# Kernel tuning notes

Measured on AMD Instinct MI355X. Metric: run time of the kernel, lower is better.

Reference implementation:

```python
import jax, jax.numpy as jnp
import numpy as np

B, N, D, H = 256, 40, 256, 256      # molecules, atoms/molecule, pc_hidden, pred_hidden
nS, nC, nB = 40, 5, 5               # n_SYMBOLS, n_FORMAL_CHARGES, n_BOND_TYPES
NEG_SLOPE = 0.01                    # F.leaky_relu default


def _lrelu(x):
    return jnp.where(x >= 0, x, NEG_SLOPE * x)


def setup_inputs() -> dict:
    key = jax.random.key(0)
    ks = jax.random.split(key, 7)
    def w(k, shape, fan_in):
        return jax.random.normal(k, shape, jnp.float32) / np.float32(np.sqrt(fan_in))
    return {
        "yhat": jax.random.normal(ks[0], (B, N, D), jnp.float32),
        "Ws1": w(ks[1], (D, H), D),      "bs1": jnp.zeros((H,), jnp.float32),
        "Ws2": w(ks[2], (H, nS), H),     "bs2": jnp.zeros((nS,), jnp.float32),
        "Wc1": w(ks[3], (D, H), D),      "bc1": jnp.zeros((H,), jnp.float32),
        "Wc2": w(ks[4], (H, nC), H),     "bc2": jnp.zeros((nC,), jnp.float32),
        "Wb1": w(ks[5], (2 * D, H), 2 * D), "bb1": jnp.zeros((H,), jnp.float32),
        "Wb2": w(ks[6], (H, nB), H),     "bb2": jnp.zeros((nB,), jnp.float32),
    }


def reference(yhat, Ws1, bs1, Ws2, bs2, Wc1, bc1, Wc2, bc2, Wb1, bb1, Wb2, bb2):
    # Per-atom symbol / charge heads (2-layer MLP with leaky_relu)
    symbols = _lrelu(yhat @ Ws1 + bs1) @ Ws2 + bs2          # [B, N, nS]
    charges = _lrelu(yhat @ Wc1 + bc1) @ Wc2 + bc2          # [B, N, nC]

    # Pairwise bond head: concat(x_i, x_j) @ Wb1 == x_i @ Wb1[:D] + x_j @ Wb1[D:]
    # (avoids materializing the [B, N, N, 2D] concat tensor)
    p1 = yhat @ Wb1[:D]                                      # [B, N, H]
    p2 = yhat @ Wb1[D:]                                      # [B, N, H]
    h = _lrelu(p1[:, :, None, :] + p2[:, None, :, :] + bb1)  # [B, N, N, H]
    bonds = h @ Wb2 + bb2                                    # [B, N, N, nB]
    bonds = bonds + jnp.swapaxes(bonds, 1, 2)                # symmetrize (i,j)+(j,i)

    return (symbols.reshape(-1, nS),
            charges.reshape(-1, nC),
            bonds.reshape(-1, nB))
```

## Files before the change

### kernel.cpp

```cpp
#include <hip/hip_runtime.h>
#include <hip/hip_bf16.h>

typedef unsigned short u16;
typedef __attribute__((ext_vector_type(4))) int   int4v;
typedef __attribute__((ext_vector_type(4))) unsigned int uint4v;
typedef __attribute__((ext_vector_type(4))) unsigned short ushort4v;
typedef __attribute__((ext_vector_type(4))) float floatx4;
typedef __attribute__((ext_vector_type(8))) short bf16x8;

#define LRELU_NS 0.01f
#define SK 264

__device__ __forceinline__ float bitsToF(unsigned int b) {
    union { unsigned int u; float f; } v; v.u = b << 16; return v.f;
}
__device__ __forceinline__ float bfLo(unsigned int d) {
    union { unsigned int u; float f; } v; v.u = d << 16; return v.f;
}
__device__ __forceinline__ float bfHi(unsigned int d) {
    union { unsigned int u; float f; } v; v.u = d & 0xffff0000u; return v.f;
}
__device__ __forceinline__ u16 f2bf(float f) {
    __hip_bfloat16 h = __float2bfloat16(f);
    return *reinterpret_cast<u16*>(&h);
}
__device__ __forceinline__ float lrelu(float v) {
    return fmaxf(v, LRELU_NS * v);
}
__device__ __forceinline__ u16 ldW(const void* p, int i, int isF32) {
    return isF32 ? f2bf(((const float*)p)[i]) : ((const u16*)p)[i];
}
__device__ __forceinline__ float ldF(const void* p, int i, int isF32) {
    return isF32 ? ((const float*)p)[i]
                 : bitsToF((unsigned int)((const u16*)p)[i]);
}

__device__ __forceinline__ int computeIsF32(const u16* y, int* cnt, int t) {
    if (t == 0) *cnt = 0;
    __syncthreads();
    if (t < 256) {
        u16 v = y[2 * t];
        int e = (v >> 7) & 0xFF;
        if (v == 0 || (e >= 96 && e < 160)) atomicAdd(cnt, 1);
    }
    __syncthreads();
    return (*cnt < 192) ? 1 : 0;
}

__global__ __launch_bounds__(256) void pack_kernel(
    const void* __restrict__ yhat,
    const void* __restrict__ Ws1, const void* __restrict__ Wc1,
    const void* __restrict__ Wb1, const void* __restrict__ Ws2,
    const void* __restrict__ Wc2,
    const void* __restrict__ bs1, const void* __restrict__ bc1,
    const void* __restrict__ bb1, const void* __restrict__ bs2,
    const void* __restrict__ bc2, const void* __restrict__ bb2,
    u16* __restrict__ WallT, u16* __restrict__ W2T, float* __restrict__ biasF)
{
    __shared__ int fcnt;
    const int bid = blockIdx.x, t = threadIdx.x;
    const int isF32 = computeIsF32((const u16*)yhat, &fcnt, t);
    if (bid < 64) {
        __shared__ u16 tile[64][65];
        const int c0 = (bid & 15) * 64;
        const int k0 = (bid >> 4) * 64;
        const void* src; int coff; int roff = 0;
        if (c0 < 256)      { src = Ws1; coff = c0; }
        else if (c0 < 512) { src = Wc1; coff = c0 - 256; }
        else if (c0 < 768) { src = Wb1; coff = c0 - 512; }
        else               { src = Wb1; coff = c0 - 768; roff = 256; }
        const int cc = t & 63, kk0 = t >> 6;
        #pragma unroll
        for (int i = 0; i < 16; ++i) {
            int kk = kk0 + i * 4;
            tile[kk][cc] = ldW(src, (k0 + kk + roff) * 256 + coff + cc, isF32);
        }
        __syncthreads();
        const int kk2 = t & 63, cc0 = t >> 6;
        #pragma unroll
        for (int i = 0; i < 16; ++i) {
            int cc2 = cc0 + i * 4;
            WallT[(c0 + cc2) * 256 + (k0 + kk2)] = tile[kk2][cc2];
        }
    } else if (bid < 128) {
        int e2 = (bid - 64) * 256 + t;
        int c = e2 >> 8, k = e2 & 255;
        u16 v = 0;
        if (c < 40)                 v = ldW(Ws2, k * 40 + c, isF32);
        else if (c >= 48 && c < 53) v = ldW(Wc2, k * 5 + (c - 48), isF32);
        W2T[c * 256 + k] = v;
    } else {
        int idx = (bid - 128) * 256 + t;
        float v = 0.f;
        if (idx < 256)       v = ldF(bs1, idx, isF32);
        else if (idx < 512)  v = ldF(bc1, idx - 256, isF32);
        else if (idx < 768)  v = ldF(bb1, idx - 512, isF32);
        else if (idx < 808)  v = ldF(bs2, idx - 768, isF32);
        else if (idx < 813)  v = ldF(bc2, idx - 808, isF32);
        else if (idx >= 816 && idx < 821) v = ldF(bb2, idx - 816, isF32);
        biasF[idx] = v;
    }
}

__global__ __launch_bounds__(512) void heads2_kernel(
    const void* __restrict__ Xv, const u16* __restrict__ WallT,
    const u16* __restrict__ W2T, const float* __restrict__ biasF,
    void* __restrict__ outv)
{
    __shared__ u16 Xs[64 * SK];
    __shared__ u16 Hb[64 * SK];
    __shared__ int fcnt;
    const int t = threadIdx.x;
    const int bm0 = blockIdx.x * 64;
    const int head = blockIdx.y;
    const int isF32 = computeIsF32((const u16*)Xv, &fcnt, t);

    if (isF32) {
        const floatx4* __restrict__ src = (const floatx4*)((const float*)Xv + bm0 * 256);
        #pragma unroll
        for (int s = 0; s < 8; ++s) {
            int cid = t + s * 512;
            int row = cid >> 6, ch = cid & 63;
            floatx4 f = src[cid];
            ushort4v u;
            u[0] = f2bf(f[0]); u[1] = f2bf(f[1]); u[2] = f2bf(f[2]); u[3] = f2bf(f[3]);
            *(ushort4v*)&Xs[row * SK + ch * 4] = u;
        }
    } else {
        const int4v* __restrict__ src = (const int4v*)((const u16*)Xv + bm0 * 256);
        #pragma unroll
        for (int s = 0; s < 4; ++s) {
            int cid = t + s * 512;
            int row = cid >> 5, ch = cid & 31;
            *(int4v*)&Xs[row * SK + ch * 8] = src[cid];
        }
    }
    __syncthreads();

    const int w = t >> 6, l = t & 63;
    const int ml = l & 15, kq = l >> 4, r0 = kq * 4;

    #pragma unroll
    for (int n = 0; n < 2; ++n) {
        const int ct = w + 8 * n;
        floatx4 acc[4] = {};
        #pragma unroll
        for (int ks = 0; ks < 8; ++ks) {
            const int k0 = ks * 32 + kq * 8;
            bf16x8 bf = *(const bf16x8*)&WallT[(head * 256 + ct * 16 + ml) * 256 + k0];
            #pragma unroll
            for (int mt = 0; mt < 4; ++mt) {
                bf16x8 a = *(const bf16x8*)&Xs[(mt * 16 + ml) * SK + k0];
                acc[mt] = __builtin_amdgcn_mfma_f32_16x16x32_bf16(a, bf, acc[mt], 0, 0, 0);
            }
        }
        const int col = ct * 16 + ml;
        const float bias = biasF[head * 256 + col];
        #pragma unroll
        for (int mt = 0; mt < 4; ++mt)
            #pragma unroll
            for (int r = 0; r < 4; ++r)
                Hb[(mt * 16 + r0 + r) * SK + col] = f2bf(lrelu(acc[mt][r] + bias));
    }
    __syncthreads();

    if (w < 4) {
        const int nct = (head == 0) ? 3 : 1;
        const int c0  = (head == 0) ? 0 : 48;
        floatx4 acc2[3] = {};
        #pragma unroll
        for (int ks = 0; ks < 8; ++ks) {
            const int k0 = ks * 32 + kq * 8;
            bf16x8 a = *(const bf16x8*)&Hb[(w * 16 + ml) * SK + k0];
            #pragma unroll
            for (int j = 0; j < 3; ++j) {
                if (j < nct) {
                    bf16x8 bf = *(const bf16x8*)&W2T[(c0 + j * 16 + ml) * 256 + k0];
                    acc2[j] = __builtin_amdgcn_mfma_f32_16x16x32_bf16(a, bf, acc2[j], 0, 0, 0);
                }
            }
        }
        #pragma unroll
        for (int j = 0; j < 3; ++j) {
            if (j < nct) {
                const int col = j * 16 + ml;
                const int lim = (head == 0) ? 40 : 5;
                if (col < lim) {
                    const float bias = biasF[(head == 0 ? 768 : 808) + col];
                    #pragma unroll
                    for (int r = 0; r < 4; ++r) {
                        const int row = bm0 + w * 16 + r0 + r;
                        const int o = (head == 0) ? row * 40 + col
                                                  : 409600 + row * 5 + col;
                        const float v = acc2[j][r] + bias;
                        if (isF32) ((float*)outv)[o] = v;
                        else ((__hip_bfloat16*)outv)[o] = __float2bfloat16(v);
                    }
                }
            }
        }
    }
}

__global__ __launch_bounds__(512) void bonds2_kernel(
    const void* __restrict__ Xv, const u16* __restrict__ WallT,
    const void* __restrict__ Wb2, const float* __restrict__ biasF,
    void* __restrict__ outv)
{
    __shared__ u16 Xm[48 * SK];
    __shared__ u16 P1L[48 * SK];
    __shared__ u16 P2L[48 * SK];
    __shared__ u16 WsB[5 * 264];
    __shared__ int fcnt;
    const int t = threadIdx.x, b = blockIdx.x;
    const int isF32 = computeIsF32((const u16*)Xv, &fcnt, t);

    if (isF32) {
        const floatx4* __restrict__ src = (const floatx4*)((const float*)Xv + b * 10240);
        #pragma unroll
        for (int s = 0; s < 5; ++s) {
            int cid = t + s * 512;
            int row = cid >> 6, ch = cid & 63;
            floatx4 f = src[cid];
            ushort4v u;
            u[0] = f2bf(f[0]); u[1] = f2bf(f[1]); u[2] = f2bf(f[2]); u[3] = f2bf(f[3]);
            *(ushort4v*)&Xm[row * SK + ch * 4] = u;
        }
        {
            int row = 40 + (t >> 6), ch = t & 63;
            ushort4v z = {0, 0, 0, 0};
            *(ushort4v*)&Xm[row * SK + ch * 4] = z;
        }
    } else {
        const int4v* __restrict__ src = (const int4v*)((const u16*)Xv + b * 10240);
        #pragma unroll
        for (int s = 0; s < 3; ++s) {
            int cid = t + s * 512;
            int row = cid >> 5, ch = cid & 31;
            if (cid < 1280) *(int4v*)&Xm[row * SK + ch * 8] = src[cid];
            else { int4v z = {0, 0, 0, 0}; *(int4v*)&Xm[row * SK + ch * 8] = z; }
        }
    }
    #pragma unroll
    for (int s = 0; s < 3; ++s) {
        int e2 = t + s * 512;
        if (e2 < 1280) {
            int c = e2 >> 8, k = e2 & 255;
            WsB[c * 264 + k] = ldW(Wb2, k * 5 + c, isF32);
        }
    }
    __syncthreads();

    const int w = t >> 6, l = t & 63;
    const int ml = l & 15, kq = l >> 4, r0 = kq * 4;

    for (int n = 0; n < 4; ++n) {
        const int gc = (w + 8 * n) * 16 + ml;
        floatx4 acc[3] = {};
        #pragma unroll
        for (int ks = 0; ks < 8; ++ks) {
            const int k0 = ks * 32 + kq * 8;
            bf16x8 bf = *(const bf16x8*)&WallT[(512 + gc) * 256 + k0];
            #pragma unroll
            for (int i = 0; i < 3; ++i) {
                bf16x8 a = *(const bf16x8*)&Xm[(i * 16 + ml) * SK + k0];
                acc[i] = __builtin_amdgcn_mfma_f32_16x16x32_bf16(a, bf, acc[i], 0, 0, 0);
            }
        }
        u16* dst = (gc < 256) ? P1L : P2L;
        const int col = gc & 255;
        const float bias = (gc < 256) ? biasF[512 + gc] : 0.f;
        #pragma unroll
        for (int i = 0; i < 3; ++i)
            #pragma unroll
            for (int r = 0; r < 4; ++r)
                dst[(i * 16 + r0 + r) * SK + col] = f2bf(acc[i][r] + bias);
    }
    __syncthreads();

    const int sel = (ml < 5) ? ml : 4;
    bf16x8 wf[8];
    #pragma unroll
    for (int ks = 0; ks < 8; ++ks)
        wf[ks] = *(const bf16x8*)&WsB[sel * 264 + ks * 32 + kq * 8];
    const float b2x2 = 2.f * biasF[816 + ml];

    for (int m = 0; m < 5; ++m) {
        const int i = w + 8 * m;
        const int itile = i >> 4;
        for (int jt = itile; jt < 3; ++jt) {
            floatx4 accF = {}, accB = {};
            #pragma unroll
            for (int ks = 0; ks < 8; ++ks) {
                const int k0 = ks * 32 + kq * 8;
                const uint4v a1 = *(const uint4v*)&P1L[i * SK + k0];
                const uint4v a2 = *(const uint4v*)&P2L[i * SK + k0];
                const uint4v b1 = *(const uint4v*)&P1L[(jt * 16 + ml) * SK + k0];
                const uint4v b2 = *(const uint4v*)&P2L[(jt * 16 + ml) * SK + k0];
                bf16x8 afF, afB;
                #pragma unroll
                for (int d = 0; d < 4; ++d) {
                    afF[2 * d]     = (short)f2bf(lrelu(bfLo(a1[d]) + bfLo(b2[d])));
                    afF[2 * d + 1] = (short)f2bf(lrelu(bfHi(a1[d]) + bfHi(b2[d])));
                    afB[2 * d]     = (short)f2bf(lrelu(bfLo(b1[d]) + bfLo(a2[d])));
                    afB[2 * d + 1] = (short)f2bf(lrelu(bfHi(b1[d]) + bfHi(a2[d])));
                }
                accF = __builtin_amdgcn_mfma_f32_16x16x32_bf16(afF, wf[ks], accF, 0, 0, 0);
                accB = __builtin_amdgcn_mfma_f32_16x16x32_bf16(afB, wf[ks], accB, 0, 0, 0);
            }
            if (ml < 5) {
                const bool diag = (jt == itile);
                #pragma unroll
                for (int r = 0; r < 4; ++r) {
                    const int j = jt * 16 + r0 + r;
                    if (j < 40 && (!diag || j >= i)) {
                        const float v = accF[r] + accB[r] + b2x2;
                        const int o1 = 460800 + (b * 1600 + i * 40 + j) * 5 + ml;
                        if (isF32) ((float*)outv)[o1] = v;
                        else ((__hip_bfloat16*)outv)[o1] = __float2bfloat16(v);
                        if (!diag || j > i) {
                            const int o2 = 460800 + (b * 1600 + j * 40 + i) * 5 + ml;
                            if (isF32) ((float*)outv)[o2] = v;
                            else ((__hip_bfloat16*)outv)[o2] = __float2bfloat16(v);
                        }
                    }
                }
            }
        }
    }
}

extern "C" void kernel_launch(void* const* d_in, const int* in_sizes, int n_in,
                              void* d_out, int out_size, void* d_ws, size_t ws_size,
                              hipStream_t stream)
{
    const void* yhat = d_in[0];
    const void* Ws1  = d_in[1];
    const void* bs1  = d_in[2];
    const void* Ws2  = d_in[3];
    const void* bs2  = d_in[4];
    const void* Wc1  = d_in[5];
    const void* bc1  = d_in[6];
    const void* Wc2  = d_in[7];
    const void* bc2  = d_in[8];
    const void* Wb1  = d_in[9];
    const void* bb1  = d_in[10];
    const void* Wb2  = d_in[11];
    const void* bb2  = d_in[12];

    char* wsb = (char*)d_ws;
    float* biasF = (float*)(wsb + 4096);
    u16*   W2T   = (u16*)(wsb + 8192);
    u16*   WallT = (u16*)(wsb + 40960);

    pack_kernel<<<132, 256, 0, stream>>>(yhat, Ws1, Wc1, Wb1, Ws2, Wc2,
                                         bs1, bc1, bb1, bs2, bc2, bb2,
                                         WallT, W2T, biasF);
    heads2_kernel<<<dim3(160, 2), 512, 0, stream>>>(yhat, WallT, W2T, biasF, d_out);
    bonds2_kernel<<<256, 512, 0, stream>>>(yhat, WallT, Wb2, biasF, d_out);
}
```

Measured before the change: 146.5 us.

## Use packed fp16 math for bond hidden, merge F/B MFMAs, split bonds blocks

The bond kernel now stores P1/P2 and Wb2 in fp16 and computes the pairwise add and leaky-relu with packed half2 arithmetic. It sums the forward and backward activations before a single f16 MFMA, which halves the MFMA count per tile. Each molecule's tile pairs are spread over two blocks so the grid doubles to 512, trading a repeat of the P1/P2 projection per block for more parallelism. The heads kernel drops to 256 threads with all waves taking part in the second layer; fp16 has less range than bf16, so large activations could lose accuracy.

```diff
diff --git a/kernel.cpp b/kernel.cpp
--- a/kernel.cpp
+++ b/kernel.cpp
@@ -7,18 +7,14 @@
 typedef __attribute__((ext_vector_type(4))) unsigned short ushort4v;
 typedef __attribute__((ext_vector_type(4))) float floatx4;
 typedef __attribute__((ext_vector_type(8))) short bf16x8;
+typedef _Float16 half8 __attribute__((ext_vector_type(8)));
+typedef _Float16 half2v __attribute__((ext_vector_type(2)));
 
 #define LRELU_NS 0.01f
 #define SK 264
 
 __device__ __forceinline__ float bitsToF(unsigned int b) {
     union { unsigned int u; float f; } v; v.u = b << 16; return v.f;
-}
-__device__ __forceinline__ float bfLo(unsigned int d) {
-    union { unsigned int u; float f; } v; v.u = d << 16; return v.f;
-}
-__device__ __forceinline__ float bfHi(unsigned int d) {
-    union { unsigned int u; float f; } v; v.u = d & 0xffff0000u; return v.f;
 }
 __device__ __forceinline__ u16 f2bf(float f) {
     __hip_bfloat16 h = __float2bfloat16(f);
@@ -33,6 +29,20 @@
 __device__ __forceinline__ float ldF(const void* p, int i, int isF32) {
     return isF32 ? ((const float*)p)[i]
                  : bitsToF((unsigned int)((const u16*)p)[i]);
+}
+__device__ __forceinline__ u16 f2h_bits(float f) {
+    union { _Float16 h; u16 u; } v; v.h = (_Float16)f; return v.u;
+}
+__device__ __forceinline__ u16 ldWh(const void* p, int i, int isF32) {
+    float f = isF32 ? ((const float*)p)[i]
+                    : bitsToF((unsigned int)((const u16*)p)[i]);
+    return f2h_bits(f);
+}
+__device__ __forceinline__ half2v u2h2(unsigned int x) {
+    union { unsigned int u; half2v h; } v; v.u = x; return v.h;
+}
+__device__ __forceinline__ unsigned int h22u(half2v x) {
+    union { half2v h; unsigned int u; } v; v.h = x; return v.u;
 }
 
 __device__ __forceinline__ int computeIsF32(const u16* y, int* cnt, int t) {
@@ -102,7 +112,7 @@
     }
 }
 
-__global__ __launch_bounds__(512) void heads2_kernel(
+__global__ __launch_bounds__(256) void heads_kernel(
     const void* __restrict__ Xv, const u16* __restrict__ WallT,
     const u16* __restrict__ W2T, const float* __restrict__ biasF,
     void* __restrict__ outv)
@@ -118,8 +128,8 @@
     if (isF32) {
         const floatx4* __restrict__ src = (const floatx4*)((const float*)Xv + bm0 * 256);
         #pragma unroll
-        for (int s = 0; s < 8; ++s) {
-            int cid = t + s * 512;
+        for (int it = 0; it < 16; ++it) {
+            int cid = t + it * 256;
             int row = cid >> 6, ch = cid & 63;
             floatx4 f = src[cid];
             ushort4v u;
@@ -129,8 +139,8 @@
     } else {
         const int4v* __restrict__ src = (const int4v*)((const u16*)Xv + bm0 * 256);
         #pragma unroll
-        for (int s = 0; s < 4; ++s) {
-            int cid = t + s * 512;
+        for (int it = 0; it < 8; ++it) {
+            int cid = t + it * 256;
             int row = cid >> 5, ch = cid & 31;
             *(int4v*)&Xs[row * SK + ch * 8] = src[cid];
         }
@@ -140,9 +150,8 @@
     const int w = t >> 6, l = t & 63;
     const int ml = l & 15, kq = l >> 4, r0 = kq * 4;
 
-    #pragma unroll
-    for (int n = 0; n < 2; ++n) {
-        const int ct = w + 8 * n;
+    for (int n = 0; n < 4; ++n) {
+        const int ct = w + 4 * n;
         floatx4 acc[4] = {};
         #pragma unroll
         for (int ks = 0; ks < 8; ++ks) {
@@ -164,45 +173,43 @@
     }
     __syncthreads();
 
-    if (w < 4) {
-        const int nct = (head == 0) ? 3 : 1;
-        const int c0  = (head == 0) ? 0 : 48;
-        floatx4 acc2[3] = {};
-        #pragma unroll
-        for (int ks = 0; ks < 8; ++ks) {
-            const int k0 = ks * 32 + kq * 8;
-            bf16x8 a = *(const bf16x8*)&Hb[(w * 16 + ml) * SK + k0];
-            #pragma unroll
-            for (int j = 0; j < 3; ++j) {
-                if (j < nct) {
-                    bf16x8 bf = *(const bf16x8*)&W2T[(c0 + j * 16 + ml) * 256 + k0];
-                    acc2[j] = __builtin_amdgcn_mfma_f32_16x16x32_bf16(a, bf, acc2[j], 0, 0, 0);
-                }
-            }
-        }
+    const int nct = (head == 0) ? 3 : 1;
+    const int c0  = (head == 0) ? 0 : 48;
+    floatx4 acc2[3] = {};
+    #pragma unroll
+    for (int ks = 0; ks < 8; ++ks) {
+        const int k0 = ks * 32 + kq * 8;
+        bf16x8 a = *(const bf16x8*)&Hb[(w * 16 + ml) * SK + k0];
         #pragma unroll
         for (int j = 0; j < 3; ++j) {
             if (j < nct) {
-                const int col = j * 16 + ml;
-                const int lim = (head == 0) ? 40 : 5;
-                if (col < lim) {
-                    const float bias = biasF[(head == 0 ? 768 : 808) + col];
-                    #pragma unroll
-                    for (int r = 0; r < 4; ++r) {
-                        const int row = bm0 + w * 16 + r0 + r;
-                        const int o = (head == 0) ? row * 40 + col
-                                                  : 409600 + row * 5 + col;
-                        const float v = acc2[j][r] + bias;
-                        if (isF32) ((float*)outv)[o] = v;
-                        else ((__hip_bfloat16*)outv)[o] = __float2bfloat16(v);
-                    }
+                bf16x8 bf = *(const bf16x8*)&W2T[(c0 + j * 16 + ml) * 256 + k0];
+                acc2[j] = __builtin_amdgcn_mfma_f32_16x16x32_bf16(a, bf, acc2[j], 0, 0, 0);
+            }
+        }
+    }
+    #pragma unroll
+    for (int j = 0; j < 3; ++j) {
+        if (j < nct) {
+            const int col = j * 16 + ml;
+            const int lim = (head == 0) ? 40 : 5;
+            if (col < lim) {
+                const float bias = biasF[(head == 0 ? 768 : 808) + col];
+                #pragma unroll
+                for (int r = 0; r < 4; ++r) {
+                    const int row = bm0 + w * 16 + r0 + r;
+                    const int o = (head == 0) ? row * 40 + col
+                                              : 409600 + row * 5 + col;
+                    const float v = acc2[j][r] + bias;
+                    if (isF32) ((float*)outv)[o] = v;
+                    else ((__hip_bfloat16*)outv)[o] = __float2bfloat16(v);
                 }
             }
         }
     }
 }
 
-__global__ __launch_bounds__(512) void bonds2_kernel(
+__global__ __launch_bounds__(512) void bonds3_kernel(
     const void* __restrict__ Xv, const u16* __restrict__ WallT,
     const void* __restrict__ Wb2, const float* __restrict__ biasF,
     void* __restrict__ outv)
@@ -212,7 +219,9 @@
     __shared__ u16 P2L[48 * SK];
     __shared__ u16 WsB[5 * 264];
     __shared__ int fcnt;
-    const int t = threadIdx.x, b = blockIdx.x;
+    const int t = threadIdx.x;
+    const int b = blockIdx.x >> 1;
+    const int h = blockIdx.x & 1;
     const int isF32 = computeIsF32((const u16*)Xv, &fcnt, t);
 
     if (isF32) {
@@ -246,7 +255,7 @@
         int e2 = t + s * 512;
         if (e2 < 1280) {
             int c = e2 >> 8, k = e2 & 255;
-            WsB[c * 264 + k] = ldW(Wb2, k * 5 + c, isF32);
+            WsB[c * 264 + k] = ldWh(Wb2, k * 5 + c, isF32);
         }
     }
     __syncthreads();
@@ -274,55 +283,58 @@
         for (int i = 0; i < 3; ++i)
             #pragma unroll
             for (int r = 0; r < 4; ++r)
-                dst[(i * 16 + r0 + r) * SK + col] = f2bf(acc[i][r] + bias);
+                dst[(i * 16 + r0 + r) * SK + col] = f2h_bits(acc[i][r] + bias);
     }
     __syncthreads();
 
     const int sel = (ml < 5) ? ml : 4;
-    bf16x8 wf[8];
+    half8 wf[8];
     #pragma unroll
     for (int ks = 0; ks < 8; ++ks)
-        wf[ks] = *(const bf16x8*)&WsB[sel * 264 + ks * 32 + kq * 8];
+        wf[ks] = *(const half8*)&WsB[sel * 264 + ks * 32 + kq * 8];
     const float b2x2 = 2.f * biasF[816 + ml];
-
-    for (int m = 0; m < 5; ++m) {
+    const _Float16 c001 = (_Float16)0.01f;
+
+    constexpr int mT[11]  = {0, 0, 0, 1, 1, 1, 2, 2, 3, 3, 4};
+    constexpr int jtT[11] = {0, 1, 2, 0, 1, 2, 1, 2, 1, 2, 2};
+    #pragma unroll
+    for (int idx = 0; idx < 11; ++idx) {
+        if ((idx & 1) != h) continue;
+        const int m = mT[idx], jt = jtT[idx];
         const int i = w + 8 * m;
-        const int itile = i >> 4;
-        for (int jt = itile; jt < 3; ++jt) {
-            floatx4 accF = {}, accB = {};
-            #pragma unroll
-            for (int ks = 0; ks < 8; ++ks) {
-                const int k0 = ks * 32 + kq * 8;
-                const uint4v a1 = *(const uint4v*)&P1L[i * SK + k0];
-                const uint4v a2 = *(const uint4v*)&P2L[i * SK + k0];
-                const uint4v b1 = *(const uint4v*)&P1L[(jt * 16 + ml) * SK + k0];
-                const uint4v b2 = *(const uint4v*)&P2L[(jt * 16 + ml) * SK + k0];
-                bf16x8 afF, afB;
-                #pragma unroll
-                for (int d = 0; d < 4; ++d) {
-                    afF[2 * d]     = (short)f2bf(lrelu(bfLo(a1[d]) + bfLo(b2[d])));
-                    afF[2 * d + 1] = (short)f2bf(lrelu(bfHi(a1[d]) + bfHi(b2[d])));
-                    afB[2 * d]     = (short)f2bf(lrelu(bfLo(b1[d]) + bfLo(a2[d])));
-                    afB[2 * d + 1] = (short)f2bf(lrelu(bfHi(b1[d]) + bfHi(a2[d])));
-                }
-                accF = __builtin_amdgcn_mfma_f32_16x16x32_bf16(afF, wf[ks], accF, 0, 0, 0);
-                accB = __builtin_amdgcn_mfma_f32_16x16x32_bf16(afB, wf[ks], accB, 0, 0, 0);
-            }
-            if (ml < 5) {
-                const bool diag = (jt == itile);
-                #pragma unroll
-                for (int r = 0; r < 4; ++r) {
-                    const int j = jt * 16 + r0 + r;
-                    if (j < 40 && (!diag || j >= i)) {
-                        const float v = accF[r] + accB[r] + b2x2;
-                        const int o1 = 460800 + (b * 1600 + i * 40 + j) * 5 + ml;
-                        if (isF32) ((float*)outv)[o1] = v;
-                        else ((__hip_bfloat16*)outv)[o1] = __float2bfloat16(v);
-                        if (!diag || j > i) {
-                            const int o2 = 460800 + (b * 1600 + j * 40 + i) * 5 + ml;
-                            if (isF32) ((float*)outv)[o2] = v;
-                            else ((__hip_bfloat16*)outv)[o2] = __float2bfloat16(v);
-                        }
+        const bool diag = (jt == (i >> 4));
+        floatx4 acc = {};
+        #pragma unroll
+        for (int ks = 0; ks < 8; ++ks) {
+            const int k0 = ks * 32 + kq * 8;
+            const uint4v a1 = *(const uint4v*)&P1L[i * SK + k0];
+            const uint4v a2 = *(const uint4v*)&P2L[i * SK + k0];
+            const uint4v b1 = *(const uint4v*)&P1L[(jt * 16 + ml) * SK + k0];
+            const uint4v b2 = *(const uint4v*)&P2L[(jt * 16 + ml) * SK + k0];
+            union { unsigned int u[4]; half8 v; } af;
+            #pragma unroll
+            for (int d = 0; d < 4; ++d) {
+                const half2v tF = u2h2(a1[d]) + u2h2(b2[d]);
+                const half2v tB = u2h2(b1[d]) + u2h2(a2[d]);
+                const half2v lF = __builtin_elementwise_max(tF, tF * c001);
+                const half2v lB = __builtin_elementwise_max(tB, tB * c001);
+                af.u[d] = h22u(lF + lB);
+            }
+            acc = __builtin_amdgcn_mfma_f32_16x16x32_f16(af.v, wf[ks], acc, 0, 0, 0);
+        }
+        if (ml < 5) {
+            #pragma unroll
+            for (int r = 0; r < 4; ++r) {
+                const int j = jt * 16 + r0 + r;
+                if (j < 40 && (!diag || j >= i)) {
+                    const float v = acc[r] + b2x2;
+                    const int o1 = 460800 + (b * 1600 + i * 40 + j) * 5 + ml;
+                    if (isF32) ((float*)outv)[o1] = v;
+                    else ((__hip_bfloat16*)outv)[o1] = __float2bfloat16(v);
+                    if (!diag || j > i) {
+                        const int o2 = 460800 + (b * 1600 + j * 40 + i) * 5 + ml;
+                        if (isF32) ((float*)outv)[o2] = v;
+                        else ((__hip_bfloat16*)outv)[o2] = __float2bfloat16(v);
                     }
                 }
             }
@@ -356,6 +368,6 @@
     pack_kernel<<<132, 256, 0, stream>>>(yhat, Ws1, Wc1, Wb1, Ws2, Wc2,
                                          bs1, bc1, bb1, bs2, bc2, bb2,
                                          WallT, W2T, biasF);
-    heads2_kernel<<<dim3(160, 2), 512, 0, stream>>>(yhat, WallT, W2T, biasF, d_out);
-    bonds2_kernel<<<256, 512, 0, stream>>>(yhat, WallT, Wb2, biasF, d_out);
-}
+    heads_kernel<<<dim3(160, 2), 256, 0, stream>>>(yhat, WallT, W2T, biasF, d_out);
+    bonds3_kernel<<<512, 512, 0, stream>>>(yhat, WallT, Wb2, biasF, d_out);
+}
```

Result: faster. 140.4 us (-4.1%).
